# Performance work log

Measured on AMD Instinct MI355X. Metric: run time of the kernel, lower is better.

Reference implementation:

```python
import jax, jax.numpy as jnp
import numpy as np

N, E = 100000, 1600000
F_IN, H, C = 64, 64, 40


def setup_inputs() -> dict:
    key = jax.random.key(0)
    k = jax.random.split(key, 6)
    x = jax.random.normal(k[0], (N, F_IN), jnp.float32)
    edge_index = jax.random.randint(k[1], (2, E), 0, N, jnp.int32)
    edge_weight = jax.random.uniform(k[2], (E,), jnp.float32)
    W1 = jax.random.normal(k[3], (F_IN, H), jnp.float32) / np.sqrt(F_IN)
    b1 = jnp.zeros((H,), jnp.float32)
    W2 = jax.random.normal(k[4], (H, C), jnp.float32) / np.sqrt(H)
    b2 = jnp.zeros((C,), jnp.float32)
    return {"x": x, "edge_index": edge_index, "edge_weight": edge_weight,
            "W1": W1, "b1": b1, "W2": W2, "b2": b2}


def reference(x, edge_index, edge_weight, W1, b1, W2, b2):
    # PyG GCNConv: add self-loops (weight 1), symmetric normalization
    # D^{-1/2} (A + I) D^{-1/2}, linear transform, scatter-add, bias.
    n = x.shape[0]
    src, dst = edge_index[0], edge_index[1]
    loop = jnp.arange(n, dtype=src.dtype)
    src_f = jnp.concatenate([src, loop])
    dst_f = jnp.concatenate([dst, loop])
    w_f = jnp.concatenate([edge_weight, jnp.ones((n,), edge_weight.dtype)])
    deg = jax.ops.segment_sum(w_f, dst_f, num_segments=n)
    dinv = jnp.where(deg > 0, jax.lax.rsqrt(deg), 0.0)
    norm = dinv[src_f] * w_f * dinv[dst_f]  # [E+N]

    def conv(h, W, b):
        h = h @ W                                    # [n, d_out]
        msg = h[src_f] * norm[:, None]               # gather + scale, [E+N, d_out]
        return jax.ops.segment_sum(msg, dst_f, num_segments=n) + b

    h = jax.nn.relu(conv(x, W1, b1))
    # dropout is identity in eval mode (training=False)
    h = conv(h, W2, b2)
    return jax.nn.log_softmax(h, axis=1)
```

## Files before the change

### kernel.cpp

```cpp
#include <hip/hip_runtime.h>
#include <math.h>

#define N_NODES 100000
#define N_EDGES 1600000
#define C_DIM 40
#define NGROUPS 6250

#define BSZ 256
#define NB  ((N_NODES + BSZ - 1) / BSZ)
#define EB  4096
#define NBE ((N_EDGES + EB - 1) / EB)

#define OFF_DINV 0
#define OFF_BB   100000
#define OFF_CS   100392
#define OFF_ROW  100800
#define OFF_H    200802
#define OFF_REC2 353684
#define OFF_H1P  3553684
#define OFF_H2P  6753684
#define OFF_AGG1 9953684

typedef float floatx4 __attribute__((ext_vector_type(4)));
typedef short shortx8 __attribute__((ext_vector_type(8)));

__device__ inline unsigned short f2bf(float f) {
    unsigned int u = __float_as_uint(f);
    u += 0x7FFF + ((u >> 16) & 1);
    return (unsigned short)(u >> 16);
}
__device__ inline float bf2f(unsigned short h) {
    return __uint_as_float(((unsigned int)h) << 16);
}
__device__ inline float bflo(unsigned int u) { return __uint_as_float(u << 16); }
__device__ inline float bfhi(unsigned int u) { return __uint_as_float(u & 0xFFFF0000u); }

__global__ __launch_bounds__(512) void k_hist2d(const int* __restrict__ ei,
                                                int* __restrict__ H,
                                                int* __restrict__ colsum) {
    __shared__ int bins[NB];
    int t = threadIdx.x, b = blockIdx.x;
    for (int i = t; i < NB; i += 512) bins[i] = 0;
    __syncthreads();
    int base = b * EB;
    for (int i = t; i < EB; i += 512) {
        int e = base + i;
        if (e < N_EDGES) atomicAdd(&bins[ei[N_EDGES + e] >> 8], 1);
    }
    __syncthreads();
    for (int i = t; i < NB; i += 512) {
        int c = bins[i];
        H[b * NB + i] = c;
        if (c) atomicAdd(&colsum[i], c);
    }
}

__global__ __launch_bounds__(512) void k_colscan(int* __restrict__ H,
                                                 const int* __restrict__ colsum,
                                                 int* __restrict__ bucketBase,
                                                 int* __restrict__ rowStart) {
    __shared__ int sd[512];
    __shared__ int sbase;
    int t = threadIdx.x, j = blockIdx.x;
    int p = 0;
    for (int i = t; i < j; i += 512) p += colsum[i];
    sd[t] = p;
    __syncthreads();
    for (int off = 256; off > 0; off >>= 1) {
        if (t < off) sd[t] += sd[t + off];
        __syncthreads();
    }
    if (t == 0) sbase = sd[0];
    __syncthreads();
    int base = sbase;
    if (t == 0) {
        bucketBase[j] = base;
        if (j == NB - 1) { bucketBase[NB] = base + colsum[j]; rowStart[N_NODES] = N_EDGES; }
    }
    __syncthreads();
    int val = (t < NBE) ? H[t * NB + j] : 0;
    sd[t] = val;
    __syncthreads();
    for (int off = 1; off < 512; off <<= 1) {
        int v = (t >= off) ? sd[t - off] : 0;
        __syncthreads();
        sd[t] += v;
        __syncthreads();
    }
    if (t < NBE) H[t * NB + j] = base + sd[t] - val;
}

__global__ __launch_bounds__(512) void k_scatter(const int* __restrict__ ei,
                                                 const float* __restrict__ w,
                                                 const int* __restrict__ blockBase,
                                                 int2* __restrict__ rec) {
    __shared__ int bases[NB];
    __shared__ int cur[NB];
    int t = threadIdx.x, b = blockIdx.x;
    for (int i = t; i < NB; i += 512) { bases[i] = blockBase[b * NB + i]; cur[i] = 0; }
    __syncthreads();
    int base = b * EB;
    for (int i = t; i < EB; i += 512) {
        int e = base + i;
        if (e < N_EDGES) {
            int s = ei[e], d = ei[N_EDGES + e];
            float wv = w[e];
            int bin = d >> 8;
            int pos = bases[bin] + atomicAdd(&cur[bin], 1);
            rec[pos] = make_int2(s | ((d & 255) << 17), __float_as_int(wv));
        }
    }
}

__global__ __launch_bounds__(512) void k_bsort(const int* __restrict__ bucketBase,
                                               const int2* __restrict__ rec,
                                               int2* __restrict__ rec2,
                                               float* __restrict__ dinv,
                                               int* __restrict__ rowStart) {
    __shared__ int   cnt[256];
    __shared__ float wsum[256];
    __shared__ int   cur[256];
    __shared__ int   sd[512];
    int t = threadIdx.x, b = blockIdx.x;
    if (t < 256) { cnt[t] = 0; wsum[t] = 0.f; }
    __syncthreads();
    int r0 = bucketBase[b], r1 = bucketBase[b + 1];
    for (int i = r0 + t; i < r1; i += 512) {
        int2 rv = rec[i];
        int l = (rv.x >> 17) & 255;
        atomicAdd(&cnt[l], 1);
        atomicAdd(&wsum[l], __int_as_float(rv.y));
    }
    __syncthreads();
    int val = (t < 256) ? cnt[t] : 0;
    sd[t] = val;
    __syncthreads();
    for (int off = 1; off < 512; off <<= 1) {
        int v = (t >= off) ? sd[t - off] : 0;
        __syncthreads();
        sd[t] += v;
        __syncthreads();
    }
    float dloc = 0.f;
    if (t < 256) {
        int excl = sd[t] - val;
        cur[t] = excl;
        int node = b * BSZ + t;
        dloc = rsqrtf(1.f + wsum[t]);
        if (node < N_NODES) {
            rowStart[node] = r0 + excl;
            dinv[node] = dloc;
        }
    }
    __syncthreads();
    if (t < 256) wsum[t] = dloc;
    __syncthreads();
    for (int i = r0 + t; i < r1; i += 512) {
        int2 rv = rec[i];
        int l = (rv.x >> 17) & 255;
        float cpart = __int_as_float(rv.y) * wsum[l];
        int pos = r0 + atomicAdd(&cur[l], 1);
        rec2[pos] = make_int2((rv.x & 0x1FFFF) << 7, __float_as_int(cpart));
    }
}

__global__ __launch_bounds__(256) void k_mm1(const float* __restrict__ x,
                                             const float* __restrict__ W1,
                                             const float* __restrict__ dinv,
                                             unsigned short* __restrict__ h1p) {
    int t = threadIdx.x, lane = t & 63, wv = t >> 6;
    int m = lane & 15, quad = lane >> 4;
    int wid = blockIdx.x * 4 + wv, nw = gridDim.x * 4;
    shortx8 B[2][4];
#pragma unroll
    for (int kc = 0; kc < 2; ++kc)
#pragma unroll
        for (int tt = 0; tt < 4; ++tt)
#pragma unroll
            for (int j = 0; j < 8; ++j) {
                int k = kc * 32 + quad * 8 + j;
                B[kc][tt][j] = (short)f2bf(W1[k * 64 + tt * 16 + m]);
            }
    for (int g = wid; g < NGROUPS; g += nw) {
        int n0 = g * 16;
        const float* xr = x + (long)(n0 + m) * 64 + quad * 8;
        floatx4 xa = ((const floatx4*)xr)[0];
        floatx4 xb = ((const floatx4*)(xr + 4))[0];
        floatx4 xc = ((const floatx4*)(xr + 32))[0];
        floatx4 xd = ((const floatx4*)(xr + 36))[0];
        shortx8 A0, A1;
#pragma unroll
        for (int j = 0; j < 4; ++j) {
            A0[j] = (short)f2bf(xa[j]);
            A0[4 + j] = (short)f2bf(xb[j]);
            A1[j] = (short)f2bf(xc[j]);
            A1[4 + j] = (short)f2bf(xd[j]);
        }
        floatx4 acc[4];
#pragma unroll
        for (int tt = 0; tt < 4; ++tt) {
            acc[tt] = (floatx4){0.f, 0.f, 0.f, 0.f};
            acc[tt] = __builtin_amdgcn_mfma_f32_16x16x32_bf16(A0, B[0][tt], acc[tt], 0, 0, 0);
            acc[tt] = __builtin_amdgcn_mfma_f32_16x16x32_bf16(A1, B[1][tt], acc[tt], 0, 0, 0);
        }
        floatx4 dv = ((const floatx4*)(dinv + n0 + quad * 4))[0];
#pragma unroll
        for (int reg = 0; reg < 4; ++reg) {
            int node = n0 + quad * 4 + reg;
            float d = dv[reg];
#pragma unroll
            for (int tt = 0; tt < 4; ++tt)
                h1p[(long)node * 64 + tt * 16 + m] = f2bf(acc[tt][reg] * d);
        }
    }
}

__global__ __launch_bounds__(256) void k_agg1(const int* __restrict__ rowStart,
                                              const int2* __restrict__ rec2,
                                              const float* __restrict__ dinv,
                                              const unsigned short* __restrict__ h1p,
                                              float* __restrict__ agg1) {
    __shared__ int2 cache[4][64];
    int t = threadIdx.x, lane = t & 63, wv = t >> 6;
    int node = blockIdx.x * 4 + wv;
    if (node >= N_NODES) return;
    int2* wc = cache[wv];
    wc[lane] = make_int2(0, 0);
    const char* hb = (const char*)h1p;
    int eslot = lane >> 4;
    int c = lane & 15;
    int lo = c << 3;
    float dn = dinv[node];
    float a0 = 0.f, a1 = 0.f, a2 = 0.f, a3 = 0.f;
    float b0 = 0.f, b1 = 0.f, b2v = 0.f, b3 = 0.f;
    if (eslot == 0) {
        const unsigned int* sp = (const unsigned int*)(hb + ((long)node << 7) + lo);
        unsigned int u0 = sp[0], u1 = sp[1];
        a0 = bflo(u0) * dn; a1 = bfhi(u0) * dn;
        a2 = bflo(u1) * dn; a3 = bfhi(u1) * dn;
    }
    int s0 = rowStart[node], s1 = rowStart[node + 1];
    for (int base = s0; base < s1; base += 64) {
        int idx = base + lane;
        if (idx < s1) wc[lane] = rec2[idx];
        __builtin_amdgcn_wave_barrier();
        int cnt = min(64, s1 - base);
        for (int j = 0; j < cnt; j += 20) {
            int2 e0, e1, e2, e3, e4;
            float w0, w1, w2, w3, w4;
            { int jj = j + eslot;      bool v = jj < cnt; e0 = wc[v ? jj : j]; w0 = v ? __int_as_float(e0.y) : 0.f; }
            { int jj = j + 4 + eslot;  bool v = jj < cnt; e1 = wc[v ? jj : j]; w1 = v ? __int_as_float(e1.y) : 0.f; }
            { int jj = j + 8 + eslot;  bool v = jj < cnt; e2 = wc[v ? jj : j]; w2 = v ? __int_as_float(e2.y) : 0.f; }
            { int jj = j + 12 + eslot; bool v = jj < cnt; e3 = wc[v ? jj : j]; w3 = v ? __int_as_float(e3.y) : 0.f; }
            { int jj = j + 16 + eslot; bool v = jj < cnt; e4 = wc[v ? jj : j]; w4 = v ? __int_as_float(e4.y) : 0.f; }
            uint2 q0 = *(const uint2*)(hb + e0.x + lo);
            uint2 q1 = *(const uint2*)(hb + e1.x + lo);
            uint2 q2 = *(const uint2*)(hb + e2.x + lo);
            uint2 q3 = *(const uint2*)(hb + e3.x + lo);
            uint2 q4 = *(const uint2*)(hb + e4.x + lo);
            a0 = fmaf(bflo(q0.x), w0, a0); a1 = fmaf(bfhi(q0.x), w0, a1);
            a2 = fmaf(bflo(q0.y), w0, a2); a3 = fmaf(bfhi(q0.y), w0, a3);
            b0 = fmaf(bflo(q1.x), w1, b0); b1 = fmaf(bfhi(q1.x), w1, b1);
            b2v = fmaf(bflo(q1.y), w1, b2v); b3 = fmaf(bfhi(q1.y), w1, b3);
            a0 = fmaf(bflo(q2.x), w2, a0); a1 = fmaf(bfhi(q2.x), w2, a1);
            a2 = fmaf(bflo(q2.y), w2, a2); a3 = fmaf(bfhi(q2.y), w2, a3);
            b0 = fmaf(bflo(q3.x), w3, b0); b1 = fmaf(bfhi(q3.x), w3, b1);
            b2v = fmaf(bflo(q3.y), w3, b2v); b3 = fmaf(bfhi(q3.y), w3, b3);
            a0 = fmaf(bflo(q4.x), w4, a0); a1 = fmaf(bfhi(q4.x), w4, a1);
            a2 = fmaf(bflo(q4.y), w4, a2); a3 = fmaf(bfhi(q4.y), w4, a3);
        }
        __builtin_amdgcn_wave_barrier();
    }
    a0 += b0; a1 += b1; a2 += b2v; a3 += b3;
    a0 += __shfl_xor(a0, 16, 64); a0 += __shfl_xor(a0, 32, 64);
    a1 += __shfl_xor(a1, 16, 64); a1 += __shfl_xor(a1, 32, 64);
    a2 += __shfl_xor(a2, 16, 64); a2 += __shfl_xor(a2, 32, 64);
    a3 += __shfl_xor(a3, 16, 64); a3 += __shfl_xor(a3, 32, 64);
    if (eslot == 0) {
        *(float4*)(agg1 + ((long)node << 6) + (c << 2)) = make_float4(a0, a1, a2, a3);
    }
}

__global__ __launch_bounds__(256) void k_mm2(const float* __restrict__ agg1,
                                             const float* __restrict__ b1,
                                             const float* __restrict__ W2,
                                             const float* __restrict__ dinv,
                                             unsigned short* __restrict__ h2p) {
    int t = threadIdx.x, lane = t & 63, wv = t >> 6;
    int m = lane & 15, quad = lane >> 4;
    int wid = blockIdx.x * 4 + wv, nw = gridDim.x * 4;
    shortx8 B[2][3];
#pragma unroll
    for (int kc = 0; kc < 2; ++kc)
#pragma unroll
        for (int tt = 0; tt < 3; ++tt) {
            int n = tt * 16 + m;
#pragma unroll
            for (int j = 0; j < 8; ++j) {
                int k = kc * 32 + quad * 8 + j;
                B[kc][tt][j] = (n < C_DIM) ? (short)f2bf(W2[k * C_DIM + n]) : (short)0;
            }
        }
    floatx4 ba0 = ((const floatx4*)(b1 + quad * 8))[0];
    floatx4 ba1 = ((const floatx4*)(b1 + quad * 8 + 4))[0];
    floatx4 bb0 = ((const floatx4*)(b1 + 32 + quad * 8))[0];
    floatx4 bb1 = ((const floatx4*)(b1 + 32 + quad * 8 + 4))[0];
    for (int g = wid; g < NGROUPS; g += nw) {
        int n0 = g * 16;
        const float* xr = agg1 + (long)(n0 + m) * 64 + quad * 8;
        floatx4 xa = ((const floatx4*)xr)[0];
        floatx4 xb = ((const floatx4*)(xr + 4))[0];
        floatx4 xc = ((const floatx4*)(xr + 32))[0];
        floatx4 xd = ((const floatx4*)(xr + 36))[0];
        shortx8 A0, A1;
#pragma unroll
        for (int j = 0; j < 4; ++j) {
            A0[j]     = (short)f2bf(fmaxf(xa[j] + ba0[j], 0.f));
            A0[4 + j] = (short)f2bf(fmaxf(xb[j] + ba1[j], 0.f));
            A1[j]     = (short)f2bf(fmaxf(xc[j] + bb0[j], 0.f));
            A1[4 + j] = (short)f2bf(fmaxf(xd[j] + bb1[j], 0.f));
        }
        floatx4 acc[3];
#pragma unroll
        for (int tt = 0; tt < 3; ++tt) {
            acc[tt] = (floatx4){0.f, 0.f, 0.f, 0.f};
            acc[tt] = __builtin_amdgcn_mfma_f32_16x16x32_bf16(A0, B[0][tt], acc[tt], 0, 0, 0);
            acc[tt] = __builtin_amdgcn_mfma_f32_16x16x32_bf16(A1, B[1][tt], acc[tt], 0, 0, 0);
        }
        floatx4 dv = ((const floatx4*)(dinv + n0 + quad * 4))[0];
#pragma unroll
        for (int reg = 0; reg < 4; ++reg) {
            int node = n0 + quad * 4 + reg;
            float d = dv[reg];
#pragma unroll
            for (int tt = 0; tt < 3; ++tt) {
                int col = tt * 16 + m;
                if (col < C_DIM)
                    h2p[(long)node * 64 + col] = f2bf(acc[tt][reg] * d);
            }
        }
    }
}

__global__ __launch_bounds__(256) void k_agg2(const int* __restrict__ rowStart,
                                              const int2* __restrict__ rec2,
                                              const float* __restrict__ dinv,
                                              const unsigned short* __restrict__ h2p,
                                              const float* __restrict__ b2,
                                              float* __restrict__ out) {
    __shared__ int2 cache[4][64];
    int t = threadIdx.x, lane = t & 63, wv = t >> 6;
    int node = blockIdx.x * 4 + wv;
    if (node >= N_NODES) return;
    int2* wc = cache[wv];
    wc[lane] = make_int2(0, 0);
    const char* hb = (const char*)h2p;
    int eslot = lane / 20;
    int c = lane - eslot * 20;
    bool elane = eslot < 3;
    int lo = c << 2;
    float dn = dinv[node];
    float alo0 = 0.f, ahi0 = 0.f, alo1 = 0.f, ahi1 = 0.f;
    if (eslot == 0) {
        unsigned int u = *(const unsigned int*)(hb + ((long)node << 7) + lo);
        alo0 = bflo(u) * dn;
        ahi0 = bfhi(u) * dn;
    }
    int s0 = rowStart[node], s1 = rowStart[node + 1];
    for (int base = s0; base < s1; base += 64) {
        int idx = base + lane;
        if (idx < s1) wc[lane] = rec2[idx];
        __builtin_amdgcn_wave_barrier();
        int cnt = min(64, s1 - base);
        for (int j = 0; j < cnt; j += 21) {
            int2 e0, e1, e2, e3, e4, e5, e6;
            float f0, f1, f2, f3, f4, f5, f6;
            { int jj = j + eslot;      bool v = elane && jj < cnt; e0 = wc[v ? jj : j]; f0 = v ? __int_as_float(e0.y) : 0.f; }
            { int jj = j + 3 + eslot;  bool v = elane && jj < cnt; e1 = wc[v ? jj : j]; f1 = v ? __int_as_float(e1.y) : 0.f; }
            { int jj = j + 6 + eslot;  bool v = elane && jj < cnt; e2 = wc[v ? jj : j]; f2 = v ? __int_as_float(e2.y) : 0.f; }
            { int jj = j + 9 + eslot;  bool v = elane && jj < cnt; e3 = wc[v ? jj : j]; f3 = v ? __int_as_float(e3.y) : 0.f; }
            { int jj = j + 12 + eslot; bool v = elane && jj < cnt; e4 = wc[v ? jj : j]; f4 = v ? __int_as_float(e4.y) : 0.f; }
            { int jj = j + 15 + eslot; bool v = elane && jj < cnt; e5 = wc[v ? jj : j]; f5 = v ? __int_as_float(e5.y) : 0.f; }
            { int jj = j + 18 + eslot; bool v = elane && jj < cnt; e6 = wc[v ? jj : j]; f6 = v ? __int_as_float(e6.y) : 0.f; }
            unsigned int q0 = *(const unsigned int*)(hb + e0.x + lo);
            unsigned int q1 = *(const unsigned int*)(hb + e1.x + lo);
            unsigned int q2 = *(const unsigned int*)(hb + e2.x + lo);
            unsigned int q3 = *(const unsigned int*)(hb + e3.x + lo);
            unsigned int q4 = *(const unsigned int*)(hb + e4.x + lo);
            unsigned int q5 = *(const unsigned int*)(hb + e5.x + lo);
            unsigned int q6 = *(const unsigned int*)(hb + e6.x + lo);
            alo0 = fmaf(bflo(q0), f0, alo0); ahi0 = fmaf(bfhi(q0), f0, ahi0);
            alo1 = fmaf(bflo(q1), f1, alo1); ahi1 = fmaf(bfhi(q1), f1, ahi1);
            alo0 = fmaf(bflo(q2), f2, alo0); ahi0 = fmaf(bfhi(q2), f2, ahi0);
            alo1 = fmaf(bflo(q3), f3, alo1); ahi1 = fmaf(bfhi(q3), f3, ahi1);
            alo0 = fmaf(bflo(q4), f4, alo0); ahi0 = fmaf(bfhi(q4), f4, ahi0);
            alo1 = fmaf(bflo(q5), f5, alo1); ahi1 = fmaf(bfhi(q5), f5, ahi1);
            alo0 = fmaf(bflo(q6), f6, alo0); ahi0 = fmaf(bfhi(q6), f6, ahi0);
        }
        __builtin_amdgcn_wave_barrier();
    }
    float alo = alo0 + alo1, ahi = ahi0 + ahi1;
    float t1 = __shfl(alo, lane + 20, 64), t2 = __shfl(alo, lane + 40, 64);
    float t3 = __shfl(ahi, lane + 20, 64), t4 = __shfl(ahi, lane + 40, 64);
    alo = alo + t1 + t2;
    ahi = ahi + t3 + t4;
    bool act = lane < 20;
    float2 bb = ((const float2*)b2)[c];
    float vlo = act ? alo + bb.x : -INFINITY;
    float vhi = act ? ahi + bb.y : -INFINITY;
    float m = fmaxf(vlo, vhi);
#pragma unroll
    for (int off = 16; off; off >>= 1) m = fmaxf(m, __shfl_xor(m, off, 64));
    const float LOG2E = 1.4426950408889634f;
    const float LN2   = 0.6931471805599453f;
    float exlo = act ? __builtin_amdgcn_exp2f((vlo - m) * LOG2E) : 0.f;
    float exhi = act ? __builtin_amdgcn_exp2f((vhi - m) * LOG2E) : 0.f;
    float s = exlo + exhi;
#pragma unroll
    for (int off = 16; off; off >>= 1) s += __shfl_xor(s, off, 64);
    float ls = m + __builtin_amdgcn_logf(s) * LN2;
    if (act) {
        *(float2*)(out + (long)node * C_DIM + (c << 1)) = make_float2(vlo - ls, vhi - ls);
    }
}

extern "C" void kernel_launch(void* const* d_in, const int* in_sizes, int n_in,
                              void* d_out, int out_size, void* d_ws, size_t ws_size,
                              hipStream_t stream) {
    const float* x  = (const float*)d_in[0];
    const int*   ei = (const int*)d_in[1];
    const float* w  = (const float*)d_in[2];
    const float* W1 = (const float*)d_in[3];
    const float* b1 = (const float*)d_in[4];
    const float* W2 = (const float*)d_in[5];
    const float* b2 = (const float*)d_in[6];
    float* out = (float*)d_out;

    float* wsf = (float*)d_ws;
    int*   wsi = (int*)d_ws;
    float* dinv       = wsf + OFF_DINV;
    int*   bucketBase = wsi + OFF_BB;
    int*   colsum     = wsi + OFF_CS;
    int*   rowStart   = wsi + OFF_ROW;
    int*   H          = wsi + OFF_H;
    int2*  rec2       = (int2*)(wsi + OFF_REC2);
    int2*  rec        = (int2*)(wsi + OFF_H1P);
    unsigned short* h1p = (unsigned short*)(wsi + OFF_H1P);
    unsigned short* h2p = (unsigned short*)(wsi + OFF_H2P);
    float* agg1       = wsf + OFF_AGG1;

    hipMemsetAsync(colsum, 0, NB * sizeof(int), stream);
    k_hist2d<<<NBE, 512, 0, stream>>>(ei, H, colsum);
    k_colscan<<<NB, 512, 0, stream>>>(H, colsum, bucketBase, rowStart);
    k_scatter<<<NBE, 512, 0, stream>>>(ei, w, H, rec);
    k_bsort<<<NB, 512, 0, stream>>>(bucketBase, rec, rec2, dinv, rowStart);

    k_mm1<<<512, 256, 0, stream>>>(x, W1, dinv, h1p);
    k_agg1<<<(N_NODES + 3) / 4, 256, 0, stream>>>(rowStart, rec2, dinv, h1p, agg1);

    k_mm2<<<512, 256, 0, stream>>>(agg1, b1, W2, dinv, h2p);
    k_agg2<<<(N_NODES + 3) / 4, 256, 0, stream>>>(rowStart, rec2, dinv, h2p, b2, out);
}
```

Before: 274.6 us.

## Replace two-level bucket sort CSR build with atomic counting sort; split h2 layout

The CSR construction moves from a per-block histogram, column scan, scatter and in-bucket sort to global atomic degree counting, a three-pass prefix scan, and direct atomic placement of each edge into its destination row. This drops the intermediate record buffer and the second bucket-local sort pass, at the cost of heavy global atomics on 100k counters and edge order within each row that depends on atomic timing. Separately, the layer-2 features are stored as a 32-column bf16 array plus an 8-column array instead of a padded 64-column row. This shrinks the gather footprint per edge in the second aggregation but adds a per-lane base and shift selection.

```diff
diff --git a/kernel.cpp b/kernel.cpp
--- a/kernel.cpp
+++ b/kernel.cpp
@@ -6,20 +6,20 @@
 #define C_DIM 40
 #define NGROUPS 6250
 
-#define BSZ 256
-#define NB  ((N_NODES + BSZ - 1) / BSZ)
-#define EB  4096
-#define NBE ((N_EDGES + EB - 1) / EB)
-
-#define OFF_DINV 0
-#define OFF_BB   100000
-#define OFF_CS   100392
-#define OFF_ROW  100800
-#define OFF_H    200802
-#define OFF_REC2 353684
-#define OFF_H1P  3553684
-#define OFF_H2P  6753684
-#define OFF_AGG1 9953684
+#define EGB 3125
+#define NSB 98
+
+#define OFF_DEGC 0
+#define OFF_WDEG 100000
+#define OFF_ROW  200000
+#define OFF_CUR  300004
+#define OFF_DINV 400004
+#define OFF_BS   500004
+#define OFF_REC2 500132
+#define OFF_H1P  3700132
+#define OFF_H2A  6900132
+#define OFF_H2B  8500132
+#define OFF_AGG1 8900132
 
 typedef float floatx4 __attribute__((ext_vector_type(4)));
 typedef short shortx8 __attribute__((ext_vector_type(8)));
@@ -29,138 +29,80 @@
     u += 0x7FFF + ((u >> 16) & 1);
     return (unsigned short)(u >> 16);
 }
-__device__ inline float bf2f(unsigned short h) {
-    return __uint_as_float(((unsigned int)h) << 16);
-}
 __device__ inline float bflo(unsigned int u) { return __uint_as_float(u << 16); }
 __device__ inline float bfhi(unsigned int u) { return __uint_as_float(u & 0xFFFF0000u); }
 
-__global__ __launch_bounds__(512) void k_hist2d(const int* __restrict__ ei,
-                                                int* __restrict__ H,
-                                                int* __restrict__ colsum) {
-    __shared__ int bins[NB];
-    int t = threadIdx.x, b = blockIdx.x;
-    for (int i = t; i < NB; i += 512) bins[i] = 0;
+__global__ __launch_bounds__(512) void k_deg(const int* __restrict__ ei,
+                                             const float* __restrict__ w,
+                                             int* __restrict__ degc,
+                                             float* __restrict__ wdeg) {
+    int e = blockIdx.x * 512 + threadIdx.x;
+    if (e < N_EDGES) {
+        int d = ei[N_EDGES + e];
+        atomicAdd(&degc[d], 1);
+        atomicAdd(&wdeg[d], w[e]);
+    }
+}
+
+__global__ __launch_bounds__(1024) void k_scan1(const int* __restrict__ degc,
+                                                int* __restrict__ rowStart,
+                                                int* __restrict__ blockSum) {
+    __shared__ int sd[1024];
+    int t = threadIdx.x, b = blockIdx.x, i = b * 1024 + t;
+    int v = (i < N_NODES) ? degc[i] : 0;
+    sd[t] = v;
     __syncthreads();
-    int base = b * EB;
-    for (int i = t; i < EB; i += 512) {
-        int e = base + i;
-        if (e < N_EDGES) atomicAdd(&bins[ei[N_EDGES + e] >> 8], 1);
-    }
+    for (int off = 1; off < 1024; off <<= 1) {
+        int u = (t >= off) ? sd[t - off] : 0;
+        __syncthreads();
+        sd[t] += u;
+        __syncthreads();
+    }
+    if (i < N_NODES) rowStart[i] = sd[t] - v;
+    if (t == 1023) blockSum[b] = sd[t];
+}
+
+__global__ __launch_bounds__(128) void k_scan2(int* __restrict__ blockSum) {
+    __shared__ int sd[128];
+    int t = threadIdx.x;
+    int v = (t < NSB) ? blockSum[t] : 0;
+    sd[t] = v;
     __syncthreads();
-    for (int i = t; i < NB; i += 512) {
-        int c = bins[i];
-        H[b * NB + i] = c;
-        if (c) atomicAdd(&colsum[i], c);
-    }
-}
-
-__global__ __launch_bounds__(512) void k_colscan(int* __restrict__ H,
-                                                 const int* __restrict__ colsum,
-                                                 int* __restrict__ bucketBase,
-                                                 int* __restrict__ rowStart) {
-    __shared__ int sd[512];
-    __shared__ int sbase;
-    int t = threadIdx.x, j = blockIdx.x;
-    int p = 0;
-    for (int i = t; i < j; i += 512) p += colsum[i];
-    sd[t] = p;
-    __syncthreads();
-    for (int off = 256; off > 0; off >>= 1) {
-        if (t < off) sd[t] += sd[t + off];
+    for (int off = 1; off < 128; off <<= 1) {
+        int u = (t >= off) ? sd[t - off] : 0;
         __syncthreads();
-    }
-    if (t == 0) sbase = sd[0];
-    __syncthreads();
-    int base = sbase;
-    if (t == 0) {
-        bucketBase[j] = base;
-        if (j == NB - 1) { bucketBase[NB] = base + colsum[j]; rowStart[N_NODES] = N_EDGES; }
-    }
-    __syncthreads();
-    int val = (t < NBE) ? H[t * NB + j] : 0;
-    sd[t] = val;
-    __syncthreads();
-    for (int off = 1; off < 512; off <<= 1) {
-        int v = (t >= off) ? sd[t - off] : 0;
+        sd[t] += u;
         __syncthreads();
-        sd[t] += v;
-        __syncthreads();
-    }
-    if (t < NBE) H[t * NB + j] = base + sd[t] - val;
-}
-
-__global__ __launch_bounds__(512) void k_scatter(const int* __restrict__ ei,
-                                                 const float* __restrict__ w,
-                                                 const int* __restrict__ blockBase,
-                                                 int2* __restrict__ rec) {
-    __shared__ int bases[NB];
-    __shared__ int cur[NB];
-    int t = threadIdx.x, b = blockIdx.x;
-    for (int i = t; i < NB; i += 512) { bases[i] = blockBase[b * NB + i]; cur[i] = 0; }
-    __syncthreads();
-    int base = b * EB;
-    for (int i = t; i < EB; i += 512) {
-        int e = base + i;
-        if (e < N_EDGES) {
-            int s = ei[e], d = ei[N_EDGES + e];
-            float wv = w[e];
-            int bin = d >> 8;
-            int pos = bases[bin] + atomicAdd(&cur[bin], 1);
-            rec[pos] = make_int2(s | ((d & 255) << 17), __float_as_int(wv));
-        }
-    }
-}
-
-__global__ __launch_bounds__(512) void k_bsort(const int* __restrict__ bucketBase,
-                                               const int2* __restrict__ rec,
-                                               int2* __restrict__ rec2,
-                                               float* __restrict__ dinv,
-                                               int* __restrict__ rowStart) {
-    __shared__ int   cnt[256];
-    __shared__ float wsum[256];
-    __shared__ int   cur[256];
-    __shared__ int   sd[512];
-    int t = threadIdx.x, b = blockIdx.x;
-    if (t < 256) { cnt[t] = 0; wsum[t] = 0.f; }
-    __syncthreads();
-    int r0 = bucketBase[b], r1 = bucketBase[b + 1];
-    for (int i = r0 + t; i < r1; i += 512) {
-        int2 rv = rec[i];
-        int l = (rv.x >> 17) & 255;
-        atomicAdd(&cnt[l], 1);
-        atomicAdd(&wsum[l], __int_as_float(rv.y));
-    }
-    __syncthreads();
-    int val = (t < 256) ? cnt[t] : 0;
-    sd[t] = val;
-    __syncthreads();
-    for (int off = 1; off < 512; off <<= 1) {
-        int v = (t >= off) ? sd[t - off] : 0;
-        __syncthreads();
-        sd[t] += v;
-        __syncthreads();
-    }
-    float dloc = 0.f;
-    if (t < 256) {
-        int excl = sd[t] - val;
-        cur[t] = excl;
-        int node = b * BSZ + t;
-        dloc = rsqrtf(1.f + wsum[t]);
-        if (node < N_NODES) {
-            rowStart[node] = r0 + excl;
-            dinv[node] = dloc;
-        }
-    }
-    __syncthreads();
-    if (t < 256) wsum[t] = dloc;
-    __syncthreads();
-    for (int i = r0 + t; i < r1; i += 512) {
-        int2 rv = rec[i];
-        int l = (rv.x >> 17) & 255;
-        float cpart = __int_as_float(rv.y) * wsum[l];
-        int pos = r0 + atomicAdd(&cur[l], 1);
-        rec2[pos] = make_int2((rv.x & 0x1FFFF) << 7, __float_as_int(cpart));
+    }
+    if (t < NSB) blockSum[t] = sd[t] - v;
+}
+
+__global__ __launch_bounds__(1024) void k_scan3(int* __restrict__ rowStart,
+                                                const int* __restrict__ blockSum,
+                                                int* __restrict__ cur,
+                                                const float* __restrict__ wdeg,
+                                                float* __restrict__ dinv) {
+    int t = threadIdx.x, b = blockIdx.x, i = b * 1024 + t;
+    if (i < N_NODES) {
+        int r = rowStart[i] + blockSum[b];
+        rowStart[i] = r;
+        cur[i] = r;
+        dinv[i] = rsqrtf(1.f + wdeg[i]);
+    }
+    if (i == 0) rowStart[N_NODES] = N_EDGES;
+}
+
+__global__ __launch_bounds__(512) void k_place(const int* __restrict__ ei,
+                                               const float* __restrict__ w,
+                                               int* __restrict__ cur,
+                                               const float* __restrict__ dinv,
+                                               int2* __restrict__ rec2) {
+    int e = blockIdx.x * 512 + threadIdx.x;
+    if (e < N_EDGES) {
+        int s = ei[e], d = ei[N_EDGES + e];
+        float cpart = w[e] * dinv[d];
+        int pos = atomicAdd(&cur[d], 1);
+        rec2[pos] = make_int2(s << 7, __float_as_int(cpart));
     }
 }
 
@@ -285,7 +227,8 @@
                                              const float* __restrict__ b1,
                                              const float* __restrict__ W2,
                                              const float* __restrict__ dinv,
-                                             unsigned short* __restrict__ h2p) {
+                                             unsigned short* __restrict__ h2a,
+                                             unsigned short* __restrict__ h2b) {
     int t = threadIdx.x, lane = t & 63, wv = t >> 6;
     int m = lane & 15, quad = lane >> 4;
     int wid = blockIdx.x * 4 + wv, nw = gridDim.x * 4;
@@ -332,12 +275,10 @@
         for (int reg = 0; reg < 4; ++reg) {
             int node = n0 + quad * 4 + reg;
             float d = dv[reg];
-#pragma unroll
-            for (int tt = 0; tt < 3; ++tt) {
-                int col = tt * 16 + m;
-                if (col < C_DIM)
-                    h2p[(long)node * 64 + col] = f2bf(acc[tt][reg] * d);
-            }
+            h2a[(long)node * 32 + m]      = f2bf(acc[0][reg] * d);
+            h2a[(long)node * 32 + 16 + m] = f2bf(acc[1][reg] * d);
+            if (m < 8)
+                h2b[(long)node * 8 + m]   = f2bf(acc[2][reg] * d);
         }
     }
 }
@@ -345,7 +286,8 @@
 __global__ __launch_bounds__(256) void k_agg2(const int* __restrict__ rowStart,
                                               const int2* __restrict__ rec2,
                                               const float* __restrict__ dinv,
-                                              const unsigned short* __restrict__ h2p,
+                                              const unsigned short* __restrict__ h2a,
+                                              const unsigned short* __restrict__ h2b,
                                               const float* __restrict__ b2,
                                               float* __restrict__ out) {
     __shared__ int2 cache[4][64];
@@ -354,15 +296,16 @@
     if (node >= N_NODES) return;
     int2* wc = cache[wv];
     wc[lane] = make_int2(0, 0);
-    const char* hb = (const char*)h2p;
     int eslot = lane / 20;
     int c = lane - eslot * 20;
     bool elane = eslot < 3;
-    int lo = c << 2;
+    const char* gb = (c < 16) ? (const char*)h2a : (const char*)h2b;
+    int sh = (c < 16) ? 1 : 3;
+    int lo2 = (c < 16) ? (c << 2) : ((c - 16) << 2);
     float dn = dinv[node];
     float alo0 = 0.f, ahi0 = 0.f, alo1 = 0.f, ahi1 = 0.f;
     if (eslot == 0) {
-        unsigned int u = *(const unsigned int*)(hb + ((long)node << 7) + lo);
+        unsigned int u = *(const unsigned int*)(gb + (((long)node << 7) >> sh) + lo2);
         alo0 = bflo(u) * dn;
         ahi0 = bfhi(u) * dn;
     }
@@ -382,13 +325,13 @@
             { int jj = j + 12 + eslot; bool v = elane && jj < cnt; e4 = wc[v ? jj : j]; f4 = v ? __int_as_float(e4.y) : 0.f; }
             { int jj = j + 15 + eslot; bool v = elane && jj < cnt; e5 = wc[v ? jj : j]; f5 = v ? __int_as_float(e5.y) : 0.f; }
             { int jj = j + 18 + eslot; bool v = elane && jj < cnt; e6 = wc[v ? jj : j]; f6 = v ? __int_as_float(e6.y) : 0.f; }
-            unsigned int q0 = *(const unsigned int*)(hb + e0.x + lo);
-            unsigned int q1 = *(const unsigned int*)(hb + e1.x + lo);
-            unsigned int q2 = *(const unsigned int*)(hb + e2.x + lo);
-            unsigned int q3 = *(const unsigned int*)(hb + e3.x + lo);
-            unsigned int q4 = *(const unsigned int*)(hb + e4.x + lo);
-            unsigned int q5 = *(const unsigned int*)(hb + e5.x + lo);
-            unsigned int q6 = *(const unsigned int*)(hb + e6.x + lo);
+            unsigned int q0 = *(const unsigned int*)(gb + (e0.x >> sh) + lo2);
+            unsigned int q1 = *(const unsigned int*)(gb + (e1.x >> sh) + lo2);
+            unsigned int q2 = *(const unsigned int*)(gb + (e2.x >> sh) + lo2);
+            unsigned int q3 = *(const unsigned int*)(gb + (e3.x >> sh) + lo2);
+            unsigned int q4 = *(const unsigned int*)(gb + (e4.x >> sh) + lo2);
+            unsigned int q5 = *(const unsigned int*)(gb + (e5.x >> sh) + lo2);
+            unsigned int q6 = *(const unsigned int*)(gb + (e6.x >> sh) + lo2);
             alo0 = fmaf(bflo(q0), f0, alo0); ahi0 = fmaf(bfhi(q0), f0, ahi0);
             alo1 = fmaf(bflo(q1), f1, alo1); ahi1 = fmaf(bfhi(q1), f1, ahi1);
             alo0 = fmaf(bflo(q2), f2, alo0); ahi0 = fmaf(bfhi(q2), f2, ahi0);
@@ -438,26 +381,29 @@
 
     float* wsf = (float*)d_ws;
     int*   wsi = (int*)d_ws;
-    float* dinv       = wsf + OFF_DINV;
-    int*   bucketBase = wsi + OFF_BB;
-    int*   colsum     = wsi + OFF_CS;
-    int*   rowStart   = wsi + OFF_ROW;
-    int*   H          = wsi + OFF_H;
-    int2*  rec2       = (int2*)(wsi + OFF_REC2);
-    int2*  rec        = (int2*)(wsi + OFF_H1P);
+    int*   degc     = wsi + OFF_DEGC;
+    float* wdeg     = wsf + OFF_WDEG;
+    int*   rowStart = wsi + OFF_ROW;
+    int*   cur      = wsi + OFF_CUR;
+    float* dinv     = wsf + OFF_DINV;
+    int*   blockSum = wsi + OFF_BS;
+    int2*  rec2     = (int2*)(wsi + OFF_REC2);
     unsigned short* h1p = (unsigned short*)(wsi + OFF_H1P);
-    unsigned short* h2p = (unsigned short*)(wsi + OFF_H2P);
-    float* agg1       = wsf + OFF_AGG1;
-
-    hipMemsetAsync(colsum, 0, NB * sizeof(int), stream);
-    k_hist2d<<<NBE, 512, 0, stream>>>(ei, H, colsum);
-    k_colscan<<<NB, 512, 0, stream>>>(H, colsum, bucketBase, rowStart);
-    k_scatter<<<NBE, 512, 0, stream>>>(ei, w, H, rec);
-    k_bsort<<<NB, 512, 0, stream>>>(bucketBase, rec, rec2, dinv, rowStart);
+    unsigned short* h2a = (unsigned short*)(wsi + OFF_H2A);
+    unsigned short* h2b = (unsigned short*)(wsi + OFF_H2B);
+    float* agg1     = wsf + OFF_AGG1;
+
+    hipMemsetAsync(d_ws, 0, 200000 * sizeof(int), stream);
+
+    k_deg<<<EGB, 512, 0, stream>>>(ei, w, degc, wdeg);
+    k_scan1<<<NSB, 1024, 0, stream>>>(degc, rowStart, blockSum);
+    k_scan2<<<1, 128, 0, stream>>>(blockSum);
+    k_scan3<<<NSB, 1024, 0, stream>>>(rowStart, blockSum, cur, wdeg, dinv);
+    k_place<<<EGB, 512, 0, stream>>>(ei, w, cur, dinv, rec2);
 
     k_mm1<<<512, 256, 0, stream>>>(x, W1, dinv, h1p);
     k_agg1<<<(N_NODES + 3) / 4, 256, 0, stream>>>(rowStart, rec2, dinv, h1p, agg1);
 
-    k_mm2<<<512, 256, 0, stream>>>(agg1, b1, W2, dinv, h2p);
-    k_agg2<<<(N_NODES + 3) / 4, 256, 0, stream>>>(rowStart, rec2, dinv, h2p, b2, out);
-}
+    k_mm2<<<512, 256, 0, stream>>>(agg1, b1, W2, dinv, h2a, h2b);
+    k_agg2<<<(N_NODES + 3) / 4, 256, 0, stream>>>(rowStart, rec2, dinv, h2a, h2b, b2, out);
+}
```

Result: slower. 465.4 us (+69.4%).
